# Kernel optimization log

Measured on AMD Instinct MI355X. Metric: run time of the kernel, lower is better.

## Reference

```python
import jax, jax.numpy as jnp
import numpy as np

N_TX = 100000; N_ADDR = 100000; E = 1000000
H = 4; D = 16; HID = 64; G = 128  # heads, head_dim, hidden_channels, num_graphs


def setup_inputs() -> dict:
    key = jax.random.key(0)
    ks = jax.random.split(key, 24)
    p = lambda k, shape: jax.random.normal(k, shape, dtype=jnp.float32) * 0.1
    return {
        "x_tx": jax.random.normal(ks[0], (N_TX, 65), dtype=jnp.float32),
        "x_addr": jax.random.normal(ks[1], (N_ADDR, 65), dtype=jnp.float32),
        "W_proj_tx": p(ks[2], (65, HID)), "b_proj_tx": p(ks[3], (HID,)),
        "W_proj_addr": p(ks[4], (65, HID)), "b_proj_addr": p(ks[5], (HID,)),
        "W_han_tx": p(ks[6], (HID, HID)), "b_han_tx": p(ks[7], (HID,)),
        "W_han_addr": p(ks[8], (HID, HID)), "b_han_addr": p(ks[9], (HID,)),
        "att_src_ta": p(ks[10], (H, D)), "att_dst_ta": p(ks[11], (H, D)),
        "att_src_at": p(ks[12], (H, D)), "att_dst_at": p(ks[13], (H, D)),
        "W_k": p(ks[14], (HID, HID)), "b_k": p(ks[15], (HID,)),
        "q": p(ks[16], (HID,)),
        "W_c1": p(ks[17], (HID, HID // 2)), "b_c1": p(ks[18], (HID // 2,)),
        "W_c2": p(ks[19], (HID // 2, 1)), "b_c2": p(ks[20], (1,)),
        "edge_ta": jnp.stack([jax.random.randint(ks[21], (E,), 0, N_TX),
                              jax.random.randint(ks[22], (E,), 0, N_ADDR)]).astype(jnp.int32),
        "edge_at": jnp.stack([jax.random.randint(ks[23], (E,), 0, N_ADDR),
                              jax.random.randint(jax.random.fold_in(key, 99), (E,), 0, N_TX)]).astype(jnp.int32),
        "batch_tx": jnp.sort(jax.random.randint(jax.random.fold_in(key, 7), (N_TX,), 0, G)).astype(jnp.int32),
    }


def _edge_softmax(alpha, dst, n):
    # softmax over edges grouped by destination node; alpha: [E, H]
    m = jax.ops.segment_max(alpha, dst, num_segments=n)
    e = jnp.exp(alpha - m[dst])
    s = jax.ops.segment_sum(e, dst, num_segments=n)
    return e / (s[dst] + 1e-16)


def _han_edge(x_src, x_dst, a_s, a_d, edge, n_dst):
    # x_src: [N_src, H, D], x_dst: [N_dst, H, D], a_s/a_d: [H, D]
    src, dst = edge[0], edge[1]
    alpha = (x_src * a_s).sum(-1)[src] + (x_dst * a_d).sum(-1)[dst]  # [E, H]
    alpha = jax.nn.leaky_relu(alpha, 0.2)
    alpha = _edge_softmax(alpha, dst, n_dst)
    out = jax.ops.segment_sum(x_src[src] * alpha[:, :, None], dst, num_segments=n_dst)
    return jax.nn.relu(out.reshape(n_dst, H * D))


def _group(xs, q, Wk, bk):
    # semantic attention across metapaths; xs: list of [N, F]
    out = jnp.stack(xs)  # [M, N, F]
    score = (q * jnp.tanh(out @ Wk + bk).mean(axis=1)).sum(-1)  # [M]
    attn = jax.nn.softmax(score)
    return (attn[:, None, None] * out).sum(0)


def reference(x_tx, x_addr, W_proj_tx, b_proj_tx, W_proj_addr, b_proj_addr,
              W_han_tx, b_han_tx, W_han_addr, b_han_addr,
              att_src_ta, att_dst_ta, att_src_at, att_dst_at,
              W_k, b_k, q, W_c1, b_c1, W_c2, b_c2,
              edge_ta, edge_at, batch_tx):
    # input projections per node type
    h_tx = x_tx @ W_proj_tx + b_proj_tx
    h_addr = x_addr @ W_proj_addr + b_proj_addr
    # HANConv node-type projections, reshaped to heads
    z_tx = (h_tx @ W_han_tx + b_han_tx).reshape(N_TX, H, D)
    z_addr = (h_addr @ W_han_addr + b_han_addr).reshape(N_ADDR, H, D)
    # per-edge-type gather / attention / scatter (dropout disabled: eval mode)
    out_addr = _han_edge(z_tx, z_addr, att_src_ta, att_dst_ta, edge_ta, N_ADDR)
    out_tx = _han_edge(z_addr, z_tx, att_src_at, att_dst_at, edge_at, N_TX)
    # semantic attention (single metapath per node type here)
    tx_feat = _group([out_tx], q, W_k, b_k)  # [N_TX, HID]
    _ = _group([out_addr], q, W_k, b_k)  # computed by HANConv but unused downstream
    # global mean pool over transaction nodes per graph
    cnt = jax.ops.segment_sum(jnp.ones((N_TX,), jnp.float32), batch_tx, num_segments=G)
    g = jax.ops.segment_sum(tx_feat, batch_tx, num_segments=G) / jnp.maximum(cnt, 1.0)[:, None]
    # classifier MLP
    return jax.nn.relu(g @ W_c1 + b_c1) @ W_c2 + b_c2  # [G, 1]
```

## Files before the change

kernel.cpp:

```cpp
#include <hip/hip_runtime.h>

#define N_TXN   100000
#define N_ADDRN 100000
#define NEDGE   1000000
#define NGRAPH  128

#define DSLOT   24
#define OVF_CAP 2048

#define OFF_Z     0
#define OFF_SS    6400000
#define OFF_SD    6800000
#define OFF_CSRD  7200000
#define OFF_CUR   9600000
#define OFF_OVFC  9700000
#define OFF_OVF   9700064
#define OFF_G     9704160
#define OFF_CNT   9712352

#define NGRP 8
#define DPG  12500
#define FILL_BLOCKS 2048

__global__ void init_kernel(float* __restrict__ ws) {
    int i = blockIdx.x * blockDim.x + threadIdx.x;
    if (i < N_TXN) ((int*)ws)[OFF_CUR + i] = 0;
    if (i < 64) ((int*)ws)[OFF_OVFC + i] = 0;
    if (i < NGRAPH * 64) ws[OFF_G + i] = 0.0f;
    if (i < NGRAPH) ws[OFF_CNT + i] = 0.0f;
}

#define PB 128
#define PT 512
__global__ __launch_bounds__(PT) void proj2_kernel(
    const float* __restrict__ x, int n_nodes,
    const float* __restrict__ Wp, const float* __restrict__ bp,
    const float* __restrict__ Wh, const float* __restrict__ bh,
    const float* __restrict__ att,
    float* __restrict__ z_out,
    float* __restrict__ s_out)
{
    __shared__ float Wp_s[65 * 64];
    __shared__ float Wh_s[64 * 64];
    __shared__ float xh_s[PB * 68];
    __shared__ float bp_s[64], bh_s[64], att_s[64];
    int t = threadIdx.x;

    for (int i = t; i < 65 * 64; i += PT) Wp_s[i] = Wp[i];
    for (int i = t; i < 64 * 64; i += PT) Wh_s[i] = Wh[i];
    if (t < 64) { bp_s[t] = bp[t]; bh_s[t] = bh[t]; att_s[t] = att[t]; }

    int ng = t >> 4;
    int fg = t & 15;
    const float4* Wpf = (const float4*)Wp_s;
    const float4* Whf = (const float4*)Wh_s;

    int ntiles = (n_nodes + PB - 1) / PB;
    for (int tile = blockIdx.x; tile < ntiles; tile += gridDim.x) {
        __syncthreads();
        int nb = tile * PB;
        int nrem = n_nodes - nb; if (nrem > PB) nrem = PB;
        int tot = nrem * 65;
        for (int i = t; i < tot; i += PT) {
            int n = i / 65, k = i - n * 65;
            xh_s[n * 68 + k] = x[(size_t)nb * 65 + i];
        }
        __syncthreads();

        float4 acc[4];
        float4 b4 = ((const float4*)bp_s)[fg];
        #pragma unroll
        for (int i = 0; i < 4; ++i) acc[i] = b4;
        for (int k = 0; k < 65; ++k) {
            float4 w = Wpf[k * 16 + fg];
            #pragma unroll
            for (int i = 0; i < 4; ++i) {
                float xv = xh_s[(ng * 4 + i) * 68 + k];
                acc[i].x += xv * w.x; acc[i].y += xv * w.y;
                acc[i].z += xv * w.z; acc[i].w += xv * w.w;
            }
        }
        __syncthreads();
        #pragma unroll
        for (int i = 0; i < 4; ++i)
            *(float4*)(&xh_s[(ng * 4 + i) * 68 + fg * 4]) = acc[i];
        __syncthreads();

        b4 = ((const float4*)bh_s)[fg];
        #pragma unroll
        for (int i = 0; i < 4; ++i) acc[i] = b4;
        for (int k = 0; k < 64; ++k) {
            float4 w = Whf[k * 16 + fg];
            #pragma unroll
            for (int i = 0; i < 4; ++i) {
                float hv = xh_s[(ng * 4 + i) * 68 + k];
                acc[i].x += hv * w.x; acc[i].y += hv * w.y;
                acc[i].z += hv * w.z; acc[i].w += hv * w.w;
            }
        }

        float a0 = att_s[fg * 4], a1 = att_s[fg * 4 + 1];
        float a2 = att_s[fg * 4 + 2], a3 = att_s[fg * 4 + 3];
        #pragma unroll
        for (int i = 0; i < 4; ++i) {
            int n = ng * 4 + i;
            if (z_out && n < nrem)
                ((float4*)(z_out + (size_t)(nb + n) * 64))[fg] = acc[i];
            float p = acc[i].x * a0 + acc[i].y * a1 + acc[i].z * a2 + acc[i].w * a3;
            p += __shfl_xor(p, 1);
            p += __shfl_xor(p, 2);
            if ((fg & 3) == 0 && n < nrem)
                s_out[(nb + n) * 4 + (fg >> 2)] = p;
        }
    }
}

__global__ __launch_bounds__(256) void fill_kernel(
    const int* __restrict__ e_src, const int* __restrict__ e_dst,
    int* __restrict__ cur, int* __restrict__ csrd,
    int* __restrict__ ovfc, int2* __restrict__ ovf)
{
    int grp = blockIdx.x & (NGRP - 1);
    int sl  = blockIdx.x >> 3;
    const int NSL = FILL_BLOCKS / NGRP;
    const int per = (NEDGE + NSL - 1) / NSL;
    int e0 = sl * per;
    int e1 = e0 + per; if (e1 > NEDGE) e1 = NEDGE;
    int lo = grp * DPG, hi = lo + DPG;
    for (int e = e0 + threadIdx.x; e < e1; e += 256) {
        int d = e_dst[e];
        if (d >= lo && d < hi) {
            int p = atomicAdd(&cur[d], 1);
            if (p < DSLOT) csrd[d * DSLOT + p] = e_src[e];
            else {
                int q = atomicAdd(ovfc, 1);
                if (q < OVF_CAP) ovf[q] = make_int2(d, e_src[e]);
            }
        }
    }
}

__global__ __launch_bounds__(256) void gather_kernel(
    const int* __restrict__ csrd, const int* __restrict__ cur,
    const float* __restrict__ s_src, const float* __restrict__ s_dst,
    const float* __restrict__ z, const int* __restrict__ batch,
    float* __restrict__ g, float* __restrict__ cnt)
{
    __shared__ int   se_s[16][16];
    __shared__ float w_s[16][16][4];
    __shared__ float gsum_s[16][68];
    __shared__ int   bid_s[16];
    int grpId = threadIdx.x >> 4;
    int l16 = threadIdx.x & 15;
    int grp = blockIdx.x & (NGRP - 1);
    int li  = (blockIdx.x >> 3) * 16 + grpId;
    bool valid = li < DPG;
    int dst = valid ? grp * DPG + li : 0;
    int deg = valid ? cur[dst] : 0;
    bool skip = deg > DSLOT;
    if (skip) deg = 0;
    int r0 = dst * DSLOT;
    int h = l16 >> 2;

    float4 sd = *(const float4*)(s_dst + dst * 4);
    float4 outA = make_float4(0.f, 0.f, 0.f, 0.f);
    float4 outB = make_float4(0.f, 0.f, 0.f, 0.f);
    float4 den = make_float4(0.f, 0.f, 0.f, 0.f);

    if (deg <= 16) {
        float4 a4 = make_float4(-1e30f, -1e30f, -1e30f, -1e30f);
        int s = 0;
        if (l16 < deg) {
            s = csrd[r0 + l16];
            float4 ss = *(const float4*)(s_src + s * 4);
            float a;
            a = ss.x + sd.x; a4.x = a >= 0.f ? a : 0.2f * a;
            a = ss.y + sd.y; a4.y = a >= 0.f ? a : 0.2f * a;
            a = ss.z + sd.z; a4.z = a >= 0.f ? a : 0.2f * a;
            a = ss.w + sd.w; a4.w = a >= 0.f ? a : 0.2f * a;
        }
        float4 mx = a4;
        #pragma unroll
        for (int o = 1; o < 16; o <<= 1) {
            mx.x = fmaxf(mx.x, __shfl_xor(mx.x, o));
            mx.y = fmaxf(mx.y, __shfl_xor(mx.y, o));
            mx.z = fmaxf(mx.z, __shfl_xor(mx.z, o));
            mx.w = fmaxf(mx.w, __shfl_xor(mx.w, o));
        }
        float4 w = make_float4(0.f, 0.f, 0.f, 0.f);
        if (l16 < deg) {
            w.x = __expf(a4.x - mx.x);
            w.y = __expf(a4.y - mx.y);
            w.z = __expf(a4.z - mx.z);
            w.w = __expf(a4.w - mx.w);
            den = w;
        }
        se_s[grpId][l16] = s;
        *(float4*)(&w_s[grpId][l16][0]) = w;
        #pragma unroll
        for (int o = 1; o < 16; o <<= 1) {
            den.x += __shfl_xor(den.x, o);
            den.y += __shfl_xor(den.y, o);
            den.z += __shfl_xor(den.z, o);
            den.w += __shfl_xor(den.w, o);
        }
        int ee = 0;
        for (; ee + 1 < deg; ee += 2) {
            int sa = se_s[grpId][ee];
            int sb = se_s[grpId][ee + 1];
            float wa = w_s[grpId][ee][h];
            float wb = w_s[grpId][ee + 1][h];
            float4 za = *(const float4*)(z + (size_t)sa * 64 + l16 * 4);
            float4 zb = *(const float4*)(z + (size_t)sb * 64 + l16 * 4);
            outA.x += za.x * wa; outA.y += za.y * wa;
            outA.z += za.z * wa; outA.w += za.w * wa;
            outB.x += zb.x * wb; outB.y += zb.y * wb;
            outB.z += zb.z * wb; outB.w += zb.w * wb;
        }
        if (ee < deg) {
            int sa = se_s[grpId][ee];
            float wa = w_s[grpId][ee][h];
            float4 za = *(const float4*)(z + (size_t)sa * 64 + l16 * 4);
            outA.x += za.x * wa; outA.y += za.y * wa;
            outA.z += za.z * wa; outA.w += za.w * wa;
        }
    } else {
        float4 mx = make_float4(-1e30f, -1e30f, -1e30f, -1e30f);
        for (int base = 0; base < deg; base += 16) {
            if (base + l16 < deg) {
                int s = csrd[r0 + base + l16];
                float4 ss = *(const float4*)(s_src + s * 4);
                float a;
                a = ss.x + sd.x; a = a >= 0.f ? a : 0.2f * a; mx.x = fmaxf(mx.x, a);
                a = ss.y + sd.y; a = a >= 0.f ? a : 0.2f * a; mx.y = fmaxf(mx.y, a);
                a = ss.z + sd.z; a = a >= 0.f ? a : 0.2f * a; mx.z = fmaxf(mx.z, a);
                a = ss.w + sd.w; a = a >= 0.f ? a : 0.2f * a; mx.w = fmaxf(mx.w, a);
            }
        }
        #pragma unroll
        for (int o = 1; o < 16; o <<= 1) {
            mx.x = fmaxf(mx.x, __shfl_xor(mx.x, o));
            mx.y = fmaxf(mx.y, __shfl_xor(mx.y, o));
            mx.z = fmaxf(mx.z, __shfl_xor(mx.z, o));
            mx.w = fmaxf(mx.w, __shfl_xor(mx.w, o));
        }
        for (int base = 0; base < deg; base += 16) {
            int cnt2 = deg - base; if (cnt2 > 16) cnt2 = 16;
            int s = 0;
            float4 w = make_float4(0.f, 0.f, 0.f, 0.f);
            if (l16 < cnt2) {
                s = csrd[r0 + base + l16];
                float4 ss = *(const float4*)(s_src + s * 4);
                float a;
                a = ss.x + sd.x; a = a >= 0.f ? a : 0.2f * a; w.x = __expf(a - mx.x);
                a = ss.y + sd.y; a = a >= 0.f ? a : 0.2f * a; w.y = __expf(a - mx.y);
                a = ss.z + sd.z; a = a >= 0.f ? a : 0.2f * a; w.z = __expf(a - mx.z);
                a = ss.w + sd.w; a = a >= 0.f ? a : 0.2f * a; w.w = __expf(a - mx.w);
                den.x += w.x; den.y += w.y; den.z += w.z; den.w += w.w;
            }
            se_s[grpId][l16] = s;
            *(float4*)(&w_s[grpId][l16][0]) = w;
            for (int ee = 0; ee < cnt2; ++ee) {
                int se = se_s[grpId][ee];
                float wl = w_s[grpId][ee][h];
                float4 zz = *(const float4*)(z + (size_t)se * 64 + l16 * 4);
                outA.x += zz.x * wl; outA.y += zz.y * wl;
                outA.z += zz.z * wl; outA.w += zz.w * wl;
            }
        }
        #pragma unroll
        for (int o = 1; o < 16; o <<= 1) {
            den.x += __shfl_xor(den.x, o);
            den.y += __shfl_xor(den.y, o);
            den.z += __shfl_xor(den.z, o);
            den.w += __shfl_xor(den.w, o);
        }
    }

    float denh = (h == 0) ? den.x : (h == 1) ? den.y : (h == 2) ? den.z : den.w;
    float inv = 1.0f / (denh + 1e-16f);
    float4 r;
    r.x = fmaxf((outA.x + outB.x) * inv, 0.f);
    r.y = fmaxf((outA.y + outB.y) * inv, 0.f);
    r.z = fmaxf((outA.z + outB.z) * inv, 0.f);
    r.w = fmaxf((outA.w + outB.w) * inv, 0.f);
    *(float4*)(&gsum_s[grpId][l16 * 4]) = r;
    if (l16 == 0) bid_s[grpId] = valid ? batch[dst] : -1;
    __syncthreads();

    if (threadIdx.x < 64) {
        int f = threadIdx.x;
        float run = 0.f, runc = 0.f;
        int cb = -1;
        for (int i = 0; i < 16; ++i) {
            int b = bid_s[i];
            if (b < 0) continue;
            if (b != cb) {
                if (cb >= 0) {
                    atomicAdd(&g[cb * 64 + f], run);
                    if (f == 0) atomicAdd(&cnt[cb], runc);
                }
                run = 0.f; runc = 0.f; cb = b;
            }
            run += gsum_s[i][f];
            runc += 1.f;
        }
        if (cb >= 0) {
            atomicAdd(&g[cb * 64 + f], run);
            if (f == 0) atomicAdd(&cnt[cb], runc);
        }
    }
}

__global__ __launch_bounds__(256) void cleanup_kernel(
    const int* __restrict__ csrd, const int* __restrict__ cur,
    const int* __restrict__ ovfc, const int2* __restrict__ ovf,
    const float* __restrict__ s_src, const float* __restrict__ s_dst,
    const float* __restrict__ z, const int* __restrict__ batch,
    float* __restrict__ g)
{
    int n = ovfc[0];
    if (n <= 0) return;
    if (n > OVF_CAP) n = OVF_CAP;
    __shared__ int od_s[OVF_CAP];
    __shared__ int os_s[OVF_CAP];
    __shared__ int ud_s[256];
    __shared__ int nuniq_s;
    __shared__ int el[16][64];
    int t = threadIdx.x;
    for (int i = t; i < n; i += 256) {
        int2 p = ovf[i]; od_s[i] = p.x; os_s[i] = p.y;
    }
    __syncthreads();
    if (t == 0) {
        int nu = 0;
        for (int i = 0; i < n && nu < 256; ++i) {
            int d = od_s[i]; bool dup = false;
            for (int j = 0; j < nu; ++j) if (ud_s[j] == d) { dup = true; break; }
            if (!dup) ud_s[nu++] = d;
        }
        nuniq_s = nu;
    }
    __syncthreads();
    int nuniq = nuniq_s;
    int g16 = t >> 4, l16 = t & 15, h = l16 >> 2;
    int trips = (nuniq + 15) >> 4;
    for (int tr = 0; tr < trips; ++tr) {
        int u = tr * 16 + g16;
        bool act = u < nuniq;
        int d = act ? ud_s[u] : 0;
        int deg = 0;
        if (act) { deg = cur[d]; if (deg > 64) deg = 64; }
        if (act && l16 == 0) {
            int c2 = 0;
            for (int k = 0; k < DSLOT && c2 < deg; ++k)
                el[g16][c2++] = csrd[d * DSLOT + k];
            for (int i = 0; i < n && c2 < deg; ++i)
                if (od_s[i] == d) el[g16][c2++] = os_s[i];
        }
        __syncthreads();
        float4 sd = *(const float4*)(s_dst + d * 4);
        float4 mx = make_float4(-1e30f, -1e30f, -1e30f, -1e30f);
        for (int e = l16; e < deg; e += 16) {
            int s = el[g16][e];
            float4 ss = *(const float4*)(s_src + s * 4);
            float a;
            a = ss.x + sd.x; a = a >= 0.f ? a : 0.2f * a; mx.x = fmaxf(mx.x, a);
            a = ss.y + sd.y; a = a >= 0.f ? a : 0.2f * a; mx.y = fmaxf(mx.y, a);
            a = ss.z + sd.z; a = a >= 0.f ? a : 0.2f * a; mx.z = fmaxf(mx.z, a);
            a = ss.w + sd.w; a = a >= 0.f ? a : 0.2f * a; mx.w = fmaxf(mx.w, a);
        }
        #pragma unroll
        for (int o = 1; o < 16; o <<= 1) {
            mx.x = fmaxf(mx.x, __shfl_xor(mx.x, o));
            mx.y = fmaxf(mx.y, __shfl_xor(mx.y, o));
            mx.z = fmaxf(mx.z, __shfl_xor(mx.z, o));
            mx.w = fmaxf(mx.w, __shfl_xor(mx.w, o));
        }
        float4 den = make_float4(0.f, 0.f, 0.f, 0.f);
        for (int e = l16; e < deg; e += 16) {
            int s = el[g16][e];
            float4 ss = *(const float4*)(s_src + s * 4);
            float a;
            a = ss.x + sd.x; a = a >= 0.f ? a : 0.2f * a; den.x += __expf(a - mx.x);
            a = ss.y + sd.y; a = a >= 0.f ? a : 0.2f * a; den.y += __expf(a - mx.y);
            a = ss.z + sd.z; a = a >= 0.f ? a : 0.2f * a; den.z += __expf(a - mx.z);
            a = ss.w + sd.w; a = a >= 0.f ? a : 0.2f * a; den.w += __expf(a - mx.w);
        }
        #pragma unroll
        for (int o = 1; o < 16; o <<= 1) {
            den.x += __shfl_xor(den.x, o);
            den.y += __shfl_xor(den.y, o);
            den.z += __shfl_xor(den.z, o);
            den.w += __shfl_xor(den.w, o);
        }
        float mh  = (h == 0) ? mx.x : (h == 1) ? mx.y : (h == 2) ? mx.z : mx.w;
        float sdh = (h == 0) ? sd.x : (h == 1) ? sd.y : (h == 2) ? sd.z : sd.w;
        float4 out = make_float4(0.f, 0.f, 0.f, 0.f);
        for (int ee = 0; ee < deg; ++ee) {
            int s = el[g16][ee];
            float a = s_src[s * 4 + h] + sdh;
            a = a >= 0.f ? a : 0.2f * a;
            float w = __expf(a - mh);
            float4 zz = *(const float4*)(z + (size_t)s * 64 + l16 * 4);
            out.x += zz.x * w; out.y += zz.y * w;
            out.z += zz.z * w; out.w += zz.w * w;
        }
        if (act) {
            float denh = (h == 0) ? den.x : (h == 1) ? den.y : (h == 2) ? den.z : den.w;
            float inv = 1.0f / (denh + 1e-16f);
            int b = batch[d];
            float* gp = g + b * 64 + l16 * 4;
            atomicAdd(gp + 0, fmaxf(out.x * inv, 0.f));
            atomicAdd(gp + 1, fmaxf(out.y * inv, 0.f));
            atomicAdd(gp + 2, fmaxf(out.z * inv, 0.f));
            atomicAdd(gp + 3, fmaxf(out.w * inv, 0.f));
        }
        __syncthreads();
    }
}

__global__ __launch_bounds__(128) void classifier_kernel(
    const float* __restrict__ g, const float* __restrict__ cnt,
    const float* __restrict__ W1, const float* __restrict__ b1,
    const float* __restrict__ W2, const float* __restrict__ b2,
    float* __restrict__ out)
{
    __shared__ float W1s[64 * 32];
    __shared__ float W2s[32];
    int t = threadIdx.x;
    for (int i = t; i < 64 * 32; i += 128) W1s[i] = W1[i];
    if (t < 32) W2s[t] = W2[t];
    __syncthreads();
    if (t >= NGRAPH) return;

    float c = fmaxf(cnt[t], 1.0f);
    float gm[64];
    #pragma unroll
    for (int k = 0; k < 64; ++k) gm[k] = g[t * 64 + k] / c;

    float o = b2[0];
    for (int j = 0; j < 32; ++j) {
        float acc = b1[j];
        #pragma unroll
        for (int k = 0; k < 64; ++k) acc += gm[k] * W1s[k * 32 + j];
        o += fmaxf(acc, 0.f) * W2s[j];
    }
    out[t] = o;
}

extern "C" void kernel_launch(void* const* d_in, const int* in_sizes, int n_in,
                              void* d_out, int out_size, void* d_ws, size_t ws_size,
                              hipStream_t stream)
{
    (void)in_sizes; (void)n_in; (void)out_size; (void)ws_size;

    const float* x_tx      = (const float*)d_in[0];
    const float* x_addr    = (const float*)d_in[1];
    const float* Wp_tx     = (const float*)d_in[2];
    const float* bp_tx     = (const float*)d_in[3];
    const float* Wp_ad     = (const float*)d_in[4];
    const float* bp_ad     = (const float*)d_in[5];
    const float* Wh_tx     = (const float*)d_in[6];
    const float* bh_tx     = (const float*)d_in[7];
    const float* Wh_ad     = (const float*)d_in[8];
    const float* bh_ad     = (const float*)d_in[9];
    const float* att_src_at = (const float*)d_in[12];
    const float* att_dst_at = (const float*)d_in[13];
    const float* W_c1      = (const float*)d_in[17];
    const float* b_c1      = (const float*)d_in[18];
    const float* W_c2      = (const float*)d_in[19];
    const float* b_c2      = (const float*)d_in[20];
    const int*   edge_at   = (const int*)d_in[22];
    const int*   batch_tx  = (const int*)d_in[23];

    float* ws    = (float*)d_ws;
    float* z_ad  = ws + OFF_Z;
    float* s_src = ws + OFF_SS;
    float* s_dst = ws + OFF_SD;
    int*   csrd  = (int*)ws + OFF_CSRD;
    int*   cur   = (int*)ws + OFF_CUR;
    int*   ovfc  = (int*)ws + OFF_OVFC;
    int2*  ovf   = (int2*)((int*)ws + OFF_OVF);
    float* g     = ws + OFF_G;
    float* cnt   = ws + OFF_CNT;

    const int* e_src = edge_at;
    const int* e_dst = edge_at + NEDGE;

    init_kernel<<<(N_TXN + 255) / 256, 256, 0, stream>>>(ws);

    proj2_kernel<<<512, PT, 0, stream>>>(
        x_addr, N_ADDRN, Wp_ad, bp_ad, Wh_ad, bh_ad, att_src_at, z_ad, s_src);
    proj2_kernel<<<512, PT, 0, stream>>>(
        x_tx, N_TXN, Wp_tx, bp_tx, Wh_tx, bh_tx, att_dst_at, nullptr, s_dst);

    fill_kernel<<<FILL_BLOCKS, 256, 0, stream>>>(
        e_src, e_dst, cur, csrd, ovfc, ovf);

    gather_kernel<<<8 * 782, 256, 0, stream>>>(
        csrd, cur, s_src, s_dst, z_ad, batch_tx, g, cnt);

    cleanup_kernel<<<1, 256, 0, stream>>>(
        csrd, cur, ovfc, ovf, s_src, s_dst, z_ad, batch_tx, g);

    classifier_kernel<<<1, 128, 0, stream>>>(
        g, cnt, W_c1, b_c1, W_c2, b_c2, (float*)d_out);
}
```

Before: 332.2 us.

## Fuse both projections and CSR fill into one role-split kernel; unroll gather by four

```diff
diff --git a/kernel.cpp b/kernel.cpp
--- a/kernel.cpp
+++ b/kernel.cpp
@@ -20,7 +20,11 @@
 
 #define NGRP 8
 #define DPG  12500
-#define FILL_BLOCKS 2048
+
+#define PB 128
+#define PT 512
+#define NPROJB 512
+#define NFILLB 1024
 
 __global__ void init_kernel(float* __restrict__ ws) {
     int i = blockIdx.x * blockDim.x + threadIdx.x;
@@ -30,22 +34,17 @@
     if (i < NGRAPH) ws[OFF_CNT + i] = 0.0f;
 }
 
-#define PB 128
-#define PT 512
-__global__ __launch_bounds__(PT) void proj2_kernel(
+__device__ __forceinline__ void proj_role(
     const float* __restrict__ x, int n_nodes,
     const float* __restrict__ Wp, const float* __restrict__ bp,
     const float* __restrict__ Wh, const float* __restrict__ bh,
     const float* __restrict__ att,
-    float* __restrict__ z_out,
-    float* __restrict__ s_out)
-{
-    __shared__ float Wp_s[65 * 64];
-    __shared__ float Wh_s[64 * 64];
-    __shared__ float xh_s[PB * 68];
-    __shared__ float bp_s[64], bh_s[64], att_s[64];
+    float* __restrict__ z_out, float* __restrict__ s_out,
+    int rb,
+    float* Wp_s, float* Wh_s, float* xh_s,
+    float* bp_s, float* bh_s, float* att_s)
+{
     int t = threadIdx.x;
-
     for (int i = t; i < 65 * 64; i += PT) Wp_s[i] = Wp[i];
     for (int i = t; i < 64 * 64; i += PT) Wh_s[i] = Wh[i];
     if (t < 64) { bp_s[t] = bp[t]; bh_s[t] = bh[t]; att_s[t] = att[t]; }
@@ -56,7 +55,7 @@
     const float4* Whf = (const float4*)Wh_s;
 
     int ntiles = (n_nodes + PB - 1) / PB;
-    for (int tile = blockIdx.x; tile < ntiles; tile += gridDim.x) {
+    for (int tile = rb; tile < ntiles; tile += NPROJB) {
         __syncthreads();
         int nb = tile * PB;
         int nrem = n_nodes - nb; if (nrem > PB) nrem = PB;
@@ -115,19 +114,19 @@
     }
 }
 
-__global__ __launch_bounds__(256) void fill_kernel(
+__device__ __forceinline__ void fill_role(
     const int* __restrict__ e_src, const int* __restrict__ e_dst,
     int* __restrict__ cur, int* __restrict__ csrd,
-    int* __restrict__ ovfc, int2* __restrict__ ovf)
-{
-    int grp = blockIdx.x & (NGRP - 1);
-    int sl  = blockIdx.x >> 3;
-    const int NSL = FILL_BLOCKS / NGRP;
+    int* __restrict__ ovfc, int2* __restrict__ ovf, int fb)
+{
+    int grp = fb & (NGRP - 1);
+    int sl  = fb >> 3;
+    const int NSL = NFILLB / NGRP;
     const int per = (NEDGE + NSL - 1) / NSL;
     int e0 = sl * per;
     int e1 = e0 + per; if (e1 > NEDGE) e1 = NEDGE;
     int lo = grp * DPG, hi = lo + DPG;
-    for (int e = e0 + threadIdx.x; e < e1; e += 256) {
+    for (int e = e0 + threadIdx.x; e < e1; e += PT) {
         int d = e_dst[e];
         if (d >= lo && d < hi) {
             int p = atomicAdd(&cur[d], 1);
@@ -137,6 +136,40 @@
                 if (q < OVF_CAP) ovf[q] = make_int2(d, e_src[e]);
             }
         }
+    }
+}
+
+__global__ __launch_bounds__(PT) void fused_kernel(
+    const float* __restrict__ x_ad,
+    const float* __restrict__ Wp_ad, const float* __restrict__ bp_ad,
+    const float* __restrict__ Wh_ad, const float* __restrict__ bh_ad,
+    const float* __restrict__ att_src,
+    const float* __restrict__ x_tx,
+    const float* __restrict__ Wp_tx, const float* __restrict__ bp_tx,
+    const float* __restrict__ Wh_tx, const float* __restrict__ bh_tx,
+    const float* __restrict__ att_dst,
+    float* __restrict__ z_ad, float* __restrict__ s_src,
+    float* __restrict__ s_dst,
+    const int* __restrict__ e_src, const int* __restrict__ e_dst,
+    int* __restrict__ cur, int* __restrict__ csrd,
+    int* __restrict__ ovfc, int2* __restrict__ ovf)
+{
+    __shared__ float Wp_s[65 * 64];
+    __shared__ float Wh_s[64 * 64];
+    __shared__ float xh_s[PB * 68];
+    __shared__ float bp_s[64], bh_s[64], att_s[64];
+
+    int role = blockIdx.x & 3;
+    int rb   = blockIdx.x >> 2;
+    if (role == 0) {
+        proj_role(x_ad, N_ADDRN, Wp_ad, bp_ad, Wh_ad, bh_ad, att_src,
+                  z_ad, s_src, rb, Wp_s, Wh_s, xh_s, bp_s, bh_s, att_s);
+    } else if (role == 1) {
+        proj_role(x_tx, N_TXN, Wp_tx, bp_tx, Wh_tx, bh_tx, att_dst,
+                  nullptr, s_dst, rb, Wp_s, Wh_s, xh_s, bp_s, bh_s, att_s);
+    } else {
+        fill_role(e_src, e_dst, cur, csrd, ovfc, ovf,
+                  (role - 2) * NPROJB + rb);
     }
 }
 
@@ -165,6 +198,8 @@
     float4 sd = *(const float4*)(s_dst + dst * 4);
     float4 outA = make_float4(0.f, 0.f, 0.f, 0.f);
     float4 outB = make_float4(0.f, 0.f, 0.f, 0.f);
+    float4 outC = make_float4(0.f, 0.f, 0.f, 0.f);
+    float4 outD = make_float4(0.f, 0.f, 0.f, 0.f);
     float4 den = make_float4(0.f, 0.f, 0.f, 0.f);
 
     if (deg <= 16) {
@@ -205,19 +240,25 @@
             den.w += __shfl_xor(den.w, o);
         }
         int ee = 0;
-        for (; ee + 1 < deg; ee += 2) {
-            int sa = se_s[grpId][ee];
-            int sb = se_s[grpId][ee + 1];
-            float wa = w_s[grpId][ee][h];
-            float wb = w_s[grpId][ee + 1][h];
+        for (; ee + 3 < deg; ee += 4) {
+            int sa = se_s[grpId][ee],     sb = se_s[grpId][ee + 1];
+            int sc = se_s[grpId][ee + 2], sdd = se_s[grpId][ee + 3];
+            float wa = w_s[grpId][ee][h],     wb = w_s[grpId][ee + 1][h];
+            float wc = w_s[grpId][ee + 2][h], wd = w_s[grpId][ee + 3][h];
             float4 za = *(const float4*)(z + (size_t)sa * 64 + l16 * 4);
             float4 zb = *(const float4*)(z + (size_t)sb * 64 + l16 * 4);
+            float4 zc = *(const float4*)(z + (size_t)sc * 64 + l16 * 4);
+            float4 zd = *(const float4*)(z + (size_t)sdd * 64 + l16 * 4);
             outA.x += za.x * wa; outA.y += za.y * wa;
             outA.z += za.z * wa; outA.w += za.w * wa;
             outB.x += zb.x * wb; outB.y += zb.y * wb;
             outB.z += zb.z * wb; outB.w += zb.w * wb;
-        }
-        if (ee < deg) {
+            outC.x += zc.x * wc; outC.y += zc.y * wc;
+            outC.z += zc.z * wc; outC.w += zc.w * wc;
+            outD.x += zd.x * wd; outD.y += zd.y * wd;
+            outD.z += zd.z * wd; outD.w += zd.w * wd;
+        }
+        for (; ee < deg; ++ee) {
             int sa = se_s[grpId][ee];
             float wa = w_s[grpId][ee][h];
             float4 za = *(const float4*)(z + (size_t)sa * 64 + l16 * 4);
@@ -280,10 +321,10 @@
     float denh = (h == 0) ? den.x : (h == 1) ? den.y : (h == 2) ? den.z : den.w;
     float inv = 1.0f / (denh + 1e-16f);
     float4 r;
-    r.x = fmaxf((outA.x + outB.x) * inv, 0.f);
-    r.y = fmaxf((outA.y + outB.y) * inv, 0.f);
-    r.z = fmaxf((outA.z + outB.z) * inv, 0.f);
-    r.w = fmaxf((outA.w + outB.w) * inv, 0.f);
+    r.x = fmaxf((outA.x + outB.x + outC.x + outD.x) * inv, 0.f);
+    r.y = fmaxf((outA.y + outB.y + outC.y + outD.y) * inv, 0.f);
+    r.z = fmaxf((outA.z + outB.z + outC.z + outD.z) * inv, 0.f);
+    r.w = fmaxf((outA.w + outB.w + outC.w + outD.w) * inv, 0.f);
     *(float4*)(&gsum_s[grpId][l16 * 4]) = r;
     if (l16 == 0) bid_s[grpId] = valid ? batch[dst] : -1;
     __syncthreads();
@@ -490,12 +531,10 @@
 
     init_kernel<<<(N_TXN + 255) / 256, 256, 0, stream>>>(ws);
 
-    proj2_kernel<<<512, PT, 0, stream>>>(
-        x_addr, N_ADDRN, Wp_ad, bp_ad, Wh_ad, bh_ad, att_src_at, z_ad, s_src);
-    proj2_kernel<<<512, PT, 0, stream>>>(
-        x_tx, N_TXN, Wp_tx, bp_tx, Wh_tx, bh_tx, att_dst_at, nullptr, s_dst);
-
-    fill_kernel<<<FILL_BLOCKS, 256, 0, stream>>>(
+    fused_kernel<<<NPROJB * 2 + NFILLB, PT, 0, stream>>>(
+        x_addr, Wp_ad, bp_ad, Wh_ad, bh_ad, att_src_at,
+        x_tx, Wp_tx, bp_tx, Wh_tx, bh_tx, att_dst_at,
+        z_ad, s_src, s_dst,
         e_src, e_dst, cur, csrd, ovfc, ovf);
 
     gather_kernel<<<8 * 782, 256, 0, stream>>>(
```

After: 314.9 us. 5.2% less time.
